# Kernel optimization log

Measured on AMD Instinct MI355X. Metric: run time of the kernel, lower is better.

## Reference

```python
import jax, jax.numpy as jnp
import numpy as np

EMBED_DIM = 1024
NUM_HEADS = 16
HEAD_DIM = EMBED_DIM // NUM_HEADS


def setup_inputs() -> dict:
    key = jax.random.key(0)
    k1, k2, k3, k4, k5 = jax.random.split(key, 5)
    B, S, D = 2, 2048, EMBED_DIM
    s_in = 1.0 / np.sqrt(D)
    x = jax.random.normal(k1, (B, S, D), dtype=jnp.float32)
    W_qkv = jax.random.uniform(k2, (D, 3 * D), dtype=jnp.float32, minval=-s_in, maxval=s_in)
    b_qkv = jax.random.uniform(k3, (3 * D,), dtype=jnp.float32, minval=-s_in, maxval=s_in)
    W_out = jax.random.uniform(k4, (D, D), dtype=jnp.float32, minval=-s_in, maxval=s_in)
    b_out = jax.random.uniform(k5, (D,), dtype=jnp.float32, minval=-s_in, maxval=s_in)
    return {"x": x, "W_qkv": W_qkv, "b_qkv": b_qkv, "W_out": W_out, "b_out": b_out}


def reference(x, W_qkv, b_qkv, W_out, b_out):
    B, S, D = x.shape
    H, Hd = NUM_HEADS, HEAD_DIM
    qkv = x @ W_qkv + b_qkv                      # [B,S,3D]
    qkv = qkv.reshape(B, S, 3, H, Hd)
    q = qkv[:, :, 0].transpose(0, 2, 1, 3)       # [B,H,S,Hd]
    k = qkv[:, :, 1].transpose(0, 2, 1, 3)
    v = qkv[:, :, 2].transpose(0, 2, 1, 3)
    scores = jnp.einsum('bhsd,bhtd->bhst', q, k) / jnp.sqrt(jnp.float32(Hd))
    attn = jax.nn.softmax(scores, axis=-1)       # dropout is identity in eval mode
    out = jnp.einsum('bhst,bhtd->bhsd', attn, v)
    out = out.transpose(0, 2, 1, 3).reshape(B, S, D)
    return out @ W_out + b_out
```

## Files before the change

### kernel.cpp

```cpp
#include <hip/hip_runtime.h>
#include <stdint.h>
#include <math.h>

#define EMBED 1024
#define HEADS 16
#define HDIM  64
#define SEQ   2048
#define BATCH 2

typedef __bf16 bf16x8 __attribute__((ext_vector_type(8)));
typedef float  f32x4  __attribute__((ext_vector_type(4)));
typedef unsigned short u16x8 __attribute__((ext_vector_type(8)));
typedef unsigned short u16x4 __attribute__((ext_vector_type(4)));
typedef uint32_t u32x4v __attribute__((ext_vector_type(4)));

static __device__ __forceinline__ unsigned short f2bf(float f){
  union { float f; uint32_t u; } v; v.f = f;
  uint32_t u = v.u;
  uint32_t r = (u + 0x7FFFu + ((u >> 16) & 1u)) >> 16;
  return (unsigned short)r;
}
static __device__ __forceinline__ bf16x8 as_bf(u16x8 v){ return __builtin_bit_cast(bf16x8, v); }

static __device__ __forceinline__ uint32_t pk_bf16(float a, float b){
#if defined(__has_builtin) && __has_builtin(__builtin_amdgcn_cvt_pk_bf16_f32)
  typedef __bf16 bf16x2 __attribute__((ext_vector_type(2)));
  bf16x2 p = __builtin_amdgcn_cvt_pk_bf16_f32(a, b);
  return __builtin_bit_cast(uint32_t, p);
#else
  return (uint32_t)f2bf(a) | ((uint32_t)f2bf(b) << 16);
#endif
}

static __device__ __forceinline__ float fexp2(float x){
#if defined(__has_builtin) && __has_builtin(__builtin_amdgcn_exp2f)
  return __builtin_amdgcn_exp2f(x);
#else
  return exp2f(x);
#endif
}

static __device__ __forceinline__ void stage16(const unsigned short* gp,
                                               unsigned short* lp_wave, int lane){
#if defined(__has_builtin) && __has_builtin(__builtin_amdgcn_global_load_lds)
  __builtin_amdgcn_global_load_lds((const __attribute__((address_space(1))) void*)gp,
                                   (__attribute__((address_space(3))) void*)lp_wave,
                                   16, 0, 0);
#else
  *(u16x8*)(lp_wave + lane * 8) = *(const u16x8*)gp;
#endif
}

__global__ __launch_bounds__(256) void cast_x(const float* __restrict__ in,
                                              unsigned short* __restrict__ out){
  int i = (blockIdx.x * 256 + threadIdx.x) * 4;
  float4 v = *(const float4*)(in + i);
  u16x4 o;
  o[0] = f2bf(v.x); o[1] = f2bf(v.y); o[2] = f2bf(v.z); o[3] = f2bf(v.w);
  *(u16x4*)(out + i) = o;
}

__global__ __launch_bounds__(256) void wtrans(const float* __restrict__ W,
                                              unsigned short* __restrict__ Wt,
                                              int N, int K){
  __shared__ unsigned short T[32 * 36];
  int t = threadIdx.x;
  int n0 = blockIdx.x * 32, k0 = blockIdx.y * 32;
  int kr = t >> 3, nc = (t & 7) * 4;
  float4 wv = *(const float4*)(W + (size_t)(k0 + kr) * N + n0 + nc);
  T[(nc + 0) * 36 + kr] = f2bf(wv.x);
  T[(nc + 1) * 36 + kr] = f2bf(wv.y);
  T[(nc + 2) * 36 + kr] = f2bf(wv.z);
  T[(nc + 3) * 36 + kr] = f2bf(wv.w);
  __syncthreads();
  int nr = t >> 3, kc = (t & 7) * 4;
  *(u16x4*)(Wt + (size_t)(n0 + nr) * K + k0 + kc) = *(const u16x4*)&T[nr * 36 + kc];
}

__global__ __launch_bounds__(256) void vtrans(const unsigned short* __restrict__ V,
                                              unsigned short* __restrict__ VT){
  __shared__ unsigned short T[32 * 36];
  int t = threadIdx.x;
  int s0 = blockIdx.x * 32, d0 = blockIdx.y * 32;
  size_t base = (size_t)blockIdx.z * SEQ * HDIM;
  int sr = t >> 3, dc = (t & 7) * 4;
  u16x4 vv = *(const u16x4*)(V + base + (size_t)(s0 + sr) * HDIM + d0 + dc);
  T[(dc + 0) * 36 + sr] = vv[0];
  T[(dc + 1) * 36 + sr] = vv[1];
  T[(dc + 2) * 36 + sr] = vv[2];
  T[(dc + 3) * 36 + sr] = vv[3];
  __syncthreads();
  int dr = t >> 3, sc = (t & 7) * 4;
  int pos = (((sc >> 2) & 3) << 3) + (((sc >> 4) & 1) << 2);
  *(u16x4*)(VT + base + (size_t)(d0 + dr) * SEQ + s0 + pos) = *(const u16x4*)&T[dr * 36 + sc];
}

template<int MODE>
__global__ __launch_bounds__(256) void gemm_bf16(
    const unsigned short* __restrict__ A,
    const unsigned short* __restrict__ Bt,
    const float* __restrict__ bias,
    float* __restrict__ Cout,
    unsigned short* __restrict__ q_ws,
    unsigned short* __restrict__ k_ws,
    unsigned short* __restrict__ v_ws,
    int M, int N, int K)
{
  __shared__ unsigned short As[128 * 32];
  __shared__ unsigned short Bs[128 * 32];
  const int tid  = threadIdx.x;
  const int bm   = blockIdx.y, bn = blockIdx.x;
  const int w    = tid >> 6, lane = tid & 63;
  const int quad = lane >> 4, l16 = lane & 15;
  const int wm   = (w >> 1) * 64, wn = (w & 1) * 64;

  f32x4 acc[4][4] = {};

  for (int k0 = 0; k0 < K; k0 += 32) {
    #pragma unroll
    for (int i = 0; i < 2; i++){
      int c = w + i * 4;
      int row = c * 16 + (lane >> 2);
      int kg = (lane & 3) ^ (row & 3);
      stage16(A  + (size_t)(bm * 128 + row) * K + k0 + kg * 8, &As[c * 512], lane);
      stage16(Bt + (size_t)(bn * 128 + row) * K + k0 + kg * 8, &Bs[c * 512], lane);
    }
    __syncthreads();

    bf16x8 af[4], bfr[4];
    #pragma unroll
    for (int t = 0; t < 4; t++){
      int ra = wm + t * 16 + l16;
      int rb = wn + t * 16 + l16;
      af[t]  = as_bf(*(const u16x8*)&As[(ra << 5) + ((quad ^ (ra & 3)) << 3)]);
      bfr[t] = as_bf(*(const u16x8*)&Bs[(rb << 5) + ((quad ^ (rb & 3)) << 3)]);
    }
    #pragma unroll
    for (int mt = 0; mt < 4; mt++)
      #pragma unroll
      for (int nt = 0; nt < 4; nt++)
        acc[mt][nt] = __builtin_amdgcn_mfma_f32_16x16x32_bf16(af[mt], bfr[nt], acc[mt][nt], 0, 0, 0);
    __syncthreads();
  }

  #pragma unroll
  for (int mt = 0; mt < 4; mt++){
    #pragma unroll
    for (int nt = 0; nt < 4; nt++){
      #pragma unroll
      for (int r = 0; r < 4; r++){
        int gm = bm * 128 + wm + mt * 16 + quad * 4 + r;
        int gn = bn * 128 + wn + nt * 16 + l16;
        float val = acc[mt][nt][r] + bias[gn];
        if (MODE == 0){
          int which = gn >> 10, rem = gn & 1023;
          int h = rem >> 6, hd = rem & 63;
          int b = gm >> 11, s = gm & 2047;
          size_t off = ((size_t)(b * HEADS + h) * SEQ + s) * HDIM + hd;
          if (which == 0)      q_ws[off] = f2bf(val * 0.18033688f);
          else if (which == 1) k_ws[off] = f2bf(val);
          else                 v_ws[off] = f2bf(val);
        } else {
          Cout[(size_t)gm * N + gn] = val;
        }
      }
    }
  }
}

__global__ __launch_bounds__(256) void attn(
    const unsigned short* __restrict__ q_ws,
    const unsigned short* __restrict__ k_ws,
    const unsigned short* __restrict__ vt_ws,
    unsigned short* __restrict__ o_ws)
{
  __shared__ unsigned short Qs[128 * 64];
  __shared__ unsigned short Ks[64 * 64];
  __shared__ unsigned short VTs[64 * 64];
  const int tid  = threadIdx.x;
  const int qt   = blockIdx.x, bh = blockIdx.y;
  const int w    = tid >> 6, lane = tid & 63;
  const int quad = lane >> 4, l16 = lane & 15;
  const size_t base = (size_t)bh * SEQ * HDIM;

  #pragma unroll
  for (int i = 0; i < 4; i++){
    int c = w * 4 + i;
    int row = c * 8 + (lane >> 3);
    int kg = (lane & 7) ^ (row & 7);
    stage16(q_ws + base + (size_t)(qt * 128 + row) * HDIM + kg * 8, &Qs[c * 512], lane);
  }

  int srow[2], skg[2];
  #pragma unroll
  for (int i = 0; i < 2; i++){
    int c = w * 2 + i;
    srow[i] = c * 8 + (lane >> 3);
    skg[i]  = (lane & 7) ^ (srow[i] & 7);
  }

  #pragma unroll
  for (int i = 0; i < 2; i++){
    int c = w * 2 + i;
    stage16(k_ws  + base + (size_t)srow[i] * HDIM + skg[i] * 8, &Ks[c * 512],  lane);
    stage16(vt_ws + base + (size_t)srow[i] * SEQ + skg[i] * 8,  &VTs[c * 512], lane);
  }
  __syncthreads();

  bf16x8 bq[2][2];
  #pragma unroll
  for (int mq = 0; mq < 2; mq++){
    int row = w * 32 + mq * 16 + l16;
    #pragma unroll
    for (int ks = 0; ks < 2; ks++)
      bq[mq][ks] = as_bf(*(const u16x8*)&Qs[(row << 6) + ((((ks << 2) + quad) ^ (row & 7)) << 3)]);
  }

  f32x4 acc[2][4] = {};
  float li[2] = {0.f, 0.f};

  for (int kt = 0; kt < SEQ / 64; kt++){
    u16x8 kpre[2], vpre[2];
    if (kt < SEQ / 64 - 1){
      #pragma unroll
      for (int i = 0; i < 2; i++){
        kpre[i] = *(const u16x8*)(k_ws  + base + (size_t)((kt + 1) * 64 + srow[i]) * HDIM + skg[i] * 8);
        vpre[i] = *(const u16x8*)(vt_ws + base + (size_t)srow[i] * SEQ + (kt + 1) * 64 + skg[i] * 8);
      }
    }

    f32x4 sf[4][2] = {};
    #pragma unroll
    for (int ks = 0; ks < 2; ks++){
      #pragma unroll
      for (int nt = 0; nt < 4; nt++){
        int rk = nt * 16 + l16;
        bf16x8 ak = as_bf(*(const u16x8*)&Ks[(rk << 6) + ((((ks << 2) + quad) ^ (rk & 7)) << 3)]);
        #pragma unroll
        for (int mq = 0; mq < 2; mq++)
          sf[nt][mq] = __builtin_amdgcn_mfma_f32_16x16x32_bf16(ak, bq[mq][ks], sf[nt][mq], 0, 0, 0);
      }
    }

    #pragma unroll
    for (int nt = 0; nt < 4; nt++)
      #pragma unroll
      for (int mq = 0; mq < 2; mq++)
        #pragma unroll
        for (int r = 0; r < 4; r++)
          sf[nt][mq][r] = fexp2(sf[nt][mq][r]);
    #pragma unroll
    for (int mq = 0; mq < 2; mq++)
      #pragma unroll
      for (int nt = 0; nt < 4; nt++)
        li[mq] += (sf[nt][mq][0] + sf[nt][mq][1]) + (sf[nt][mq][2] + sf[nt][mq][3]);

    #pragma unroll
    for (int c = 0; c < 2; c++){
      bf16x8 ap[2];
      #pragma unroll
      for (int mq = 0; mq < 2; mq++){
        u32x4v aw;
        aw[0] = pk_bf16(sf[c * 2][mq][0],     sf[c * 2][mq][1]);
        aw[1] = pk_bf16(sf[c * 2][mq][2],     sf[c * 2][mq][3]);
        aw[2] = pk_bf16(sf[c * 2 + 1][mq][0], sf[c * 2 + 1][mq][1]);
        aw[3] = pk_bf16(sf[c * 2 + 1][mq][2], sf[c * 2 + 1][mq][3]);
        ap[mq] = __builtin_bit_cast(bf16x8, aw);
      }
      #pragma unroll
      for (int nt = 0; nt < 4; nt++){
        int rv = nt * 16 + l16;
        bf16x8 bv = as_bf(*(const u16x8*)&VTs[(rv << 6) + ((((c << 2) + quad) ^ (rv & 7)) << 3)]);
        #pragma unroll
        for (int mq = 0; mq < 2; mq++)
          acc[mq][nt] = __builtin_amdgcn_mfma_f32_16x16x32_bf16(ap[mq], bv, acc[mq][nt], 0, 0, 0);
      }
    }
    __syncthreads();

    if (kt < SEQ / 64 - 1){
      #pragma unroll
      for (int i = 0; i < 2; i++){
        int c = w * 2 + i;
        *(u16x8*)&Ks[c * 512 + lane * 8]  = kpre[i];
        *(u16x8*)&VTs[c * 512 + lane * 8] = vpre[i];
      }
      __syncthreads();
    }
  }

  #pragma unroll
  for (int mq = 0; mq < 2; mq++){
    li[mq] += __shfl_xor(li[mq], 16);
    li[mq] += __shfl_xor(li[mq], 32);
  }
  float inv[2] = {1.0f / li[0], 1.0f / li[1]};
  float invr[2][4];
  #pragma unroll
  for (int mq = 0; mq < 2; mq++)
    #pragma unroll
    for (int r = 0; r < 4; r++)
      invr[mq][r] = __shfl(inv[mq], quad * 4 + r);

  int b = bh >> 4, h = bh & 15;
  #pragma unroll
  for (int mq = 0; mq < 2; mq++)
    #pragma unroll
    for (int nt = 0; nt < 4; nt++)
      #pragma unroll
      for (int r = 0; r < 4; r++){
        int s = qt * 128 + w * 32 + mq * 16 + quad * 4 + r;
        int d = h * 64 + nt * 16 + l16;
        o_ws[((size_t)(b * SEQ + s)) * EMBED + d] = f2bf(acc[mq][nt][r] * invr[mq][r]);
      }
}

extern "C" void kernel_launch(void* const* d_in, const int* in_sizes, int n_in,
                              void* d_out, int out_size, void* d_ws, size_t ws_size,
                              hipStream_t stream) {
  const float* x     = (const float*)d_in[0];
  const float* W_qkv = (const float*)d_in[1];
  const float* b_qkv = (const float*)d_in[2];
  const float* W_out = (const float*)d_in[3];
  const float* b_out = (const float*)d_in[4];
  float* out = (float*)d_out;

  char* ws = (char*)d_ws;
  unsigned short* xb    = (unsigned short*)(ws);
  unsigned short* q     = (unsigned short*)(ws + ((size_t)8  << 20));
  unsigned short* k     = (unsigned short*)(ws + ((size_t)16 << 20));
  unsigned short* v     = (unsigned short*)(ws + ((size_t)24 << 20));
  unsigned short* vt    = (unsigned short*)(ws + ((size_t)32 << 20));
  unsigned short* wqkvT = (unsigned short*)(ws + ((size_t)32 << 20));
  unsigned short* woutT = (unsigned short*)(ws + ((size_t)24 << 20));
  unsigned short* o     = xb;

  cast_x<<<dim3(4096), dim3(256), 0, stream>>>(x, xb);

  wtrans<<<dim3(96, 32), dim3(256), 0, stream>>>(W_qkv, wqkvT, 3072, 1024);

  gemm_bf16<0><<<dim3(24, 32), dim3(256), 0, stream>>>(
      xb, wqkvT, b_qkv, nullptr, q, k, v, 4096, 3072, 1024);

  vtrans<<<dim3(64, 2, 32), dim3(256), 0, stream>>>(v, vt);

  wtrans<<<dim3(32, 32), dim3(256), 0, stream>>>(W_out, woutT, 1024, 1024);

  attn<<<dim3(16, 32), dim3(256), 0, stream>>>(q, k, vt, o);

  gemm_bf16<1><<<dim3(8, 32), dim3(256), 0, stream>>>(
      o, woutT, b_out, out, nullptr, nullptr, nullptr, 4096, 1024, 1024);
}
```

Measured before the change: 209.3 us.

## Fuse V transpose into QKV GEMM, double-buffer attention K/V, narrow out-proj tiles

The QKV GEMM epilogue now writes V directly in the permuted transposed layout that attention expects, which removes the separate vtrans kernel and its global round trip. The attention loop switches from register prefetch plus an LDS copy to double-buffered LDS staged directly from global memory, dropping one barrier per tile. The output projection gets its own kernel with 128x64 tiles, doubling the block count to 512 for better CU occupancy. The costs are more LDS per attention block, which may lower occupancy, and strided 8-byte stores for V.

```diff
diff --git a/kernel.cpp b/kernel.cpp
--- a/kernel.cpp
+++ b/kernel.cpp
@@ -77,33 +77,13 @@
   *(u16x4*)(Wt + (size_t)(n0 + nr) * K + k0 + kc) = *(const u16x4*)&T[nr * 36 + kc];
 }
 
-__global__ __launch_bounds__(256) void vtrans(const unsigned short* __restrict__ V,
-                                              unsigned short* __restrict__ VT){
-  __shared__ unsigned short T[32 * 36];
-  int t = threadIdx.x;
-  int s0 = blockIdx.x * 32, d0 = blockIdx.y * 32;
-  size_t base = (size_t)blockIdx.z * SEQ * HDIM;
-  int sr = t >> 3, dc = (t & 7) * 4;
-  u16x4 vv = *(const u16x4*)(V + base + (size_t)(s0 + sr) * HDIM + d0 + dc);
-  T[(dc + 0) * 36 + sr] = vv[0];
-  T[(dc + 1) * 36 + sr] = vv[1];
-  T[(dc + 2) * 36 + sr] = vv[2];
-  T[(dc + 3) * 36 + sr] = vv[3];
-  __syncthreads();
-  int dr = t >> 3, sc = (t & 7) * 4;
-  int pos = (((sc >> 2) & 3) << 3) + (((sc >> 4) & 1) << 2);
-  *(u16x4*)(VT + base + (size_t)(d0 + dr) * SEQ + s0 + pos) = *(const u16x4*)&T[dr * 36 + sc];
-}
-
-template<int MODE>
-__global__ __launch_bounds__(256) void gemm_bf16(
+__global__ __launch_bounds__(256) void gemm_qkv(
     const unsigned short* __restrict__ A,
     const unsigned short* __restrict__ Bt,
     const float* __restrict__ bias,
-    float* __restrict__ Cout,
     unsigned short* __restrict__ q_ws,
     unsigned short* __restrict__ k_ws,
-    unsigned short* __restrict__ v_ws,
+    unsigned short* __restrict__ vt_ws,
     int M, int N, int K)
 {
   __shared__ unsigned short As[128 * 32];
@@ -143,29 +123,116 @@
     __syncthreads();
   }
 
-  #pragma unroll
-  for (int mt = 0; mt < 4; mt++){
-    #pragma unroll
-    for (int nt = 0; nt < 4; nt++){
+  const int which = (bn * 128) >> 10;
+
+  if (which == 2){
+    #pragma unroll
+    for (int mt = 0; mt < 4; mt++){
+      int tpar = ((wm >> 4) + mt) & 1;
+      int gm0  = bm * 128 + wm + mt * 16 + quad * 4;
+      int b    = gm0 >> 11;
+      int s0   = gm0 & 2047;
+      int s32  = s0 & ~31;
+      int pos  = quad * 8 + tpar * 4;
+      #pragma unroll
+      for (int nt = 0; nt < 4; nt++){
+        int gn = bn * 128 + wn + nt * 16 + l16;
+        int rem = gn & 1023;
+        int h = rem >> 6, hd = rem & 63;
+        float bv = bias[gn];
+        u16x4 st;
+        uint32_t p0 = pk_bf16(acc[mt][nt][0] + bv, acc[mt][nt][1] + bv);
+        uint32_t p1 = pk_bf16(acc[mt][nt][2] + bv, acc[mt][nt][3] + bv);
+        st[0] = (unsigned short)p0; st[1] = (unsigned short)(p0 >> 16);
+        st[2] = (unsigned short)p1; st[3] = (unsigned short)(p1 >> 16);
+        size_t off = ((size_t)(b * HEADS + h) * HDIM + hd) * SEQ + s32 + pos;
+        *(u16x4*)(vt_ws + off) = st;
+      }
+    }
+  } else {
+    unsigned short* dst = (which == 0) ? q_ws : k_ws;
+    const float scale = (which == 0) ? 0.18033688f : 1.0f;
+    #pragma unroll
+    for (int mt = 0; mt < 4; mt++){
+      #pragma unroll
+      for (int nt = 0; nt < 4; nt++){
+        #pragma unroll
+        for (int r = 0; r < 4; r++){
+          int gm = bm * 128 + wm + mt * 16 + quad * 4 + r;
+          int gn = bn * 128 + wn + nt * 16 + l16;
+          int rem = gn & 1023;
+          int h = rem >> 6, hd = rem & 63;
+          int b = gm >> 11, s = gm & 2047;
+          float val = (acc[mt][nt][r] + bias[gn]) * scale;
+          dst[((size_t)(b * HEADS + h) * SEQ + s) * HDIM + hd] = f2bf(val);
+        }
+      }
+    }
+  }
+}
+
+__global__ __launch_bounds__(256) void gemm_out(
+    const unsigned short* __restrict__ A,
+    const unsigned short* __restrict__ Bt,
+    const float* __restrict__ bias,
+    float* __restrict__ Cout,
+    int M, int N, int K)
+{
+  __shared__ unsigned short As[128 * 32];
+  __shared__ unsigned short Bs[64 * 32];
+  const int tid  = threadIdx.x;
+  const int bm   = blockIdx.y, bn = blockIdx.x;
+  const int w    = tid >> 6, lane = tid & 63;
+  const int quad = lane >> 4, l16 = lane & 15;
+  const int wm   = (w >> 1) * 64, wn = (w & 1) * 32;
+
+  f32x4 acc[4][2] = {};
+
+  for (int k0 = 0; k0 < K; k0 += 32) {
+    #pragma unroll
+    for (int i = 0; i < 2; i++){
+      int c = w + i * 4;
+      int row = c * 16 + (lane >> 2);
+      int kg = (lane & 3) ^ (row & 3);
+      stage16(A + (size_t)(bm * 128 + row) * K + k0 + kg * 8, &As[c * 512], lane);
+    }
+    {
+      int c = w;
+      int row = c * 16 + (lane >> 2);
+      int kg = (lane & 3) ^ (row & 3);
+      stage16(Bt + (size_t)(bn * 64 + row) * K + k0 + kg * 8, &Bs[c * 512], lane);
+    }
+    __syncthreads();
+
+    bf16x8 af[4], bfr[2];
+    #pragma unroll
+    for (int t = 0; t < 4; t++){
+      int ra = wm + t * 16 + l16;
+      af[t] = as_bf(*(const u16x8*)&As[(ra << 5) + ((quad ^ (ra & 3)) << 3)]);
+    }
+    #pragma unroll
+    for (int t = 0; t < 2; t++){
+      int rb = wn + t * 16 + l16;
+      bfr[t] = as_bf(*(const u16x8*)&Bs[(rb << 5) + ((quad ^ (rb & 3)) << 3)]);
+    }
+    #pragma unroll
+    for (int mt = 0; mt < 4; mt++)
+      #pragma unroll
+      for (int nt = 0; nt < 2; nt++)
+        acc[mt][nt] = __builtin_amdgcn_mfma_f32_16x16x32_bf16(af[mt], bfr[nt], acc[mt][nt], 0, 0, 0);
+    __syncthreads();
+  }
+
+  #pragma unroll
+  for (int mt = 0; mt < 4; mt++)
+    #pragma unroll
+    for (int nt = 0; nt < 2; nt++)
       #pragma unroll
       for (int r = 0; r < 4; r++){
         int gm = bm * 128 + wm + mt * 16 + quad * 4 + r;
-        int gn = bn * 128 + wn + nt * 16 + l16;
-        float val = acc[mt][nt][r] + bias[gn];
-        if (MODE == 0){
-          int which = gn >> 10, rem = gn & 1023;
-          int h = rem >> 6, hd = rem & 63;
-          int b = gm >> 11, s = gm & 2047;
-          size_t off = ((size_t)(b * HEADS + h) * SEQ + s) * HDIM + hd;
-          if (which == 0)      q_ws[off] = f2bf(val * 0.18033688f);
-          else if (which == 1) k_ws[off] = f2bf(val);
-          else                 v_ws[off] = f2bf(val);
-        } else {
-          Cout[(size_t)gm * N + gn] = val;
-        }
-      }
-    }
-  }
+        int gn = bn * 64 + wn + nt * 16 + l16;
+        Cout[(size_t)gm * N + gn] = acc[mt][nt][r] + bias[gn];
+      }
 }
 
 __global__ __launch_bounds__(256) void attn(
@@ -175,8 +242,8 @@
     unsigned short* __restrict__ o_ws)
 {
   __shared__ unsigned short Qs[128 * 64];
-  __shared__ unsigned short Ks[64 * 64];
-  __shared__ unsigned short VTs[64 * 64];
+  __shared__ unsigned short Ks[2][64 * 64];
+  __shared__ unsigned short VTs[2][64 * 64];
   const int tid  = threadIdx.x;
   const int qt   = blockIdx.x, bh = blockIdx.y;
   const int w    = tid >> 6, lane = tid & 63;
@@ -202,8 +269,8 @@
   #pragma unroll
   for (int i = 0; i < 2; i++){
     int c = w * 2 + i;
-    stage16(k_ws  + base + (size_t)srow[i] * HDIM + skg[i] * 8, &Ks[c * 512],  lane);
-    stage16(vt_ws + base + (size_t)srow[i] * SEQ + skg[i] * 8,  &VTs[c * 512], lane);
+    stage16(k_ws  + base + (size_t)srow[i] * HDIM + skg[i] * 8, &Ks[0][c * 512],  lane);
+    stage16(vt_ws + base + (size_t)srow[i] * SEQ + skg[i] * 8,  &VTs[0][c * 512], lane);
   }
   __syncthreads();
 
@@ -220,12 +287,15 @@
   float li[2] = {0.f, 0.f};
 
   for (int kt = 0; kt < SEQ / 64; kt++){
-    u16x8 kpre[2], vpre[2];
+    const int cur = kt & 1;
     if (kt < SEQ / 64 - 1){
       #pragma unroll
       for (int i = 0; i < 2; i++){
-        kpre[i] = *(const u16x8*)(k_ws  + base + (size_t)((kt + 1) * 64 + srow[i]) * HDIM + skg[i] * 8);
-        vpre[i] = *(const u16x8*)(vt_ws + base + (size_t)srow[i] * SEQ + (kt + 1) * 64 + skg[i] * 8);
+        int c = w * 2 + i;
+        stage16(k_ws  + base + (size_t)((kt + 1) * 64 + srow[i]) * HDIM + skg[i] * 8,
+                &Ks[cur ^ 1][c * 512], lane);
+        stage16(vt_ws + base + (size_t)srow[i] * SEQ + (kt + 1) * 64 + skg[i] * 8,
+                &VTs[cur ^ 1][c * 512], lane);
       }
     }
 
@@ -235,7 +305,7 @@
       #pragma unroll
       for (int nt = 0; nt < 4; nt++){
         int rk = nt * 16 + l16;
-        bf16x8 ak = as_bf(*(const u16x8*)&Ks[(rk << 6) + ((((ks << 2) + quad) ^ (rk & 7)) << 3)]);
+        bf16x8 ak = as_bf(*(const u16x8*)&Ks[cur][(rk << 6) + ((((ks << 2) + quad) ^ (rk & 7)) << 3)]);
         #pragma unroll
         for (int mq = 0; mq < 2; mq++)
           sf[nt][mq] = __builtin_amdgcn_mfma_f32_16x16x32_bf16(ak, bq[mq][ks], sf[nt][mq], 0, 0, 0);
@@ -270,23 +340,13 @@
       #pragma unroll
       for (int nt = 0; nt < 4; nt++){
         int rv = nt * 16 + l16;
-        bf16x8 bv = as_bf(*(const u16x8*)&VTs[(rv << 6) + ((((c << 2) + quad) ^ (rv & 7)) << 3)]);
+        bf16x8 bv = as_bf(*(const u16x8*)&VTs[cur][(rv << 6) + ((((c << 2) + quad) ^ (rv & 7)) << 3)]);
         #pragma unroll
         for (int mq = 0; mq < 2; mq++)
           acc[mq][nt] = __builtin_amdgcn_mfma_f32_16x16x32_bf16(ap[mq], bv, acc[mq][nt], 0, 0, 0);
       }
     }
     __syncthreads();
-
-    if (kt < SEQ / 64 - 1){
-      #pragma unroll
-      for (int i = 0; i < 2; i++){
-        int c = w * 2 + i;
-        *(u16x8*)&Ks[c * 512 + lane * 8]  = kpre[i];
-        *(u16x8*)&VTs[c * 512 + lane * 8] = vpre[i];
-      }
-      __syncthreads();
-    }
   }
 
   #pragma unroll
@@ -329,25 +389,22 @@
   unsigned short* xb    = (unsigned short*)(ws);
   unsigned short* q     = (unsigned short*)(ws + ((size_t)8  << 20));
   unsigned short* k     = (unsigned short*)(ws + ((size_t)16 << 20));
-  unsigned short* v     = (unsigned short*)(ws + ((size_t)24 << 20));
-  unsigned short* vt    = (unsigned short*)(ws + ((size_t)32 << 20));
+  unsigned short* vt    = (unsigned short*)(ws + ((size_t)24 << 20));
   unsigned short* wqkvT = (unsigned short*)(ws + ((size_t)32 << 20));
-  unsigned short* woutT = (unsigned short*)(ws + ((size_t)24 << 20));
+  unsigned short* woutT = (unsigned short*)(ws + ((size_t)38 << 20));
   unsigned short* o     = xb;
 
   cast_x<<<dim3(4096), dim3(256), 0, stream>>>(x, xb);
 
   wtrans<<<dim3(96, 32), dim3(256), 0, stream>>>(W_qkv, wqkvT, 3072, 1024);
 
-  gemm_bf16<0><<<dim3(24, 32), dim3(256), 0, stream>>>(
-      xb, wqkvT, b_qkv, nullptr, q, k, v, 4096, 3072, 1024);
-
-  vtrans<<<dim3(64, 2, 32), dim3(256), 0, stream>>>(v, vt);
+  gemm_qkv<<<dim3(24, 32), dim3(256), 0, stream>>>(
+      xb, wqkvT, b_qkv, q, k, vt, 4096, 3072, 1024);
 
   wtrans<<<dim3(32, 32), dim3(256), 0, stream>>>(W_out, woutT, 1024, 1024);
 
   attn<<<dim3(16, 32), dim3(256), 0, stream>>>(q, k, vt, o);
 
-  gemm_bf16<1><<<dim3(8, 32), dim3(256), 0, stream>>>(
-      o, woutT, b_out, out, nullptr, nullptr, nullptr, 4096, 1024, 1024);
-}
+  gemm_out<<<dim3(16, 32), dim3(256), 0, stream>>>(
+      o, woutT, b_out, out, 4096, 1024, 1024);
+}
```

Result: slower. 222.5 us (+6.3%).
